# Kernel tuning notes

Hardware: AMD Instinct MI355X
Metric: run time of the kernel (lower is better)

## Reference

```python
import jax, jax.numpy as jnp
import numpy as np

TAO, M = 3, 5
C_IN, D_MODEL = 7, 512
KERNELS = D_MODEL // C_IN            # 73
LEFTOUT = D_MODEL - C_IN * KERNELS   # 1
KSIZE = 3
B, L = 32, 4096


def setup_inputs() -> dict:
    key = jax.random.key(0)
    k1, k2, k3, k4, k5 = jax.random.split(key, 5)
    x = jax.random.normal(k1, (B, L, C_IN), dtype=jnp.float32)
    fan_in = (M + 1) * KSIZE
    # kaiming_normal_(mode='fan_in', nonlinearity='leaky_relu', neg_slope=0.01)
    std = float(np.sqrt(2.0 / ((1.0 + 0.01 ** 2) * fan_in)))
    conv_w = jax.random.normal(k2, (KERNELS, M + 1, KSIZE), dtype=jnp.float32) * std
    bb = float(1.0 / np.sqrt(fan_in))  # torch default conv bias init: U(-1/sqrt(fan_in), +)
    conv_b = jax.random.uniform(k3, (KERNELS,), minval=-bb, maxval=bb, dtype=jnp.float32)
    leftout_w = jax.random.normal(k4, (LEFTOUT, M + 1, KSIZE), dtype=jnp.float32) * std
    leftout_b = jax.random.uniform(k5, (LEFTOUT,), minval=-bb, maxval=bb, dtype=jnp.float32)
    return {"x": x, "conv_w": conv_w, "conv_b": conv_b,
            "leftout_w": leftout_w, "leftout_b": leftout_b}


def _circ_conv(inp, w, b):
    # inp: [N, M+1, L]; circular padding=1, kernel 3, 'VALID' after wrap pad
    inp_c = jnp.pad(inp, ((0, 0), (0, 0), (1, 1)), mode="wrap")
    out = jax.lax.conv_general_dilated(
        inp_c, w, window_strides=(1,), padding="VALID",
        dimension_numbers=("NCH", "OIH", "NCH"))
    return out + b[None, :, None]


def reference(x, conv_w, conv_b, leftout_w, leftout_b):
    Bb, Ll, c = x.shape
    off = M * TAO
    # faithful-vector gather: for t in [off, L), take x[t - i*tao, c_], c-major then i
    idx = jnp.arange(off, Ll)[:, None] - jnp.arange(M + 1)[None, :] * TAO  # [L', M+1]
    g = x[:, idx, :]                                   # [B, L', M+1, c]
    g = jnp.transpose(g, (0, 1, 3, 2)).reshape(Bb, Ll - off, c * (M + 1))
    emb = jnp.pad(g, ((0, 0), (off, 0), (0, 0)))       # pad front of seq -> [B, L, c*(M+1)]
    # split into c chunks of (M+1) channels; fold chunk dim into batch for shared conv
    inp = emb.reshape(Bb, Ll, c, M + 1).transpose(0, 2, 3, 1).reshape(Bb * c, M + 1, Ll)
    out = _circ_conv(inp, conv_w, conv_b)              # [B*c, KERNELS, L]
    pieces = out.reshape(Bb, c * KERNELS, Ll)
    if LEFTOUT > 0:
        last = inp.reshape(Bb, c, M + 1, Ll)[:, -1]    # last chunk's conv input [B, M+1, L]
        extra = _circ_conv(last, leftout_w, leftout_b)  # [B, LEFTOUT, L]
        pieces = jnp.concatenate([pieces, extra], axis=1)
    return jnp.transpose(pieces, (0, 2, 1))            # [B, L, d_model]
```

## Files before the change

### kernel.cpp

```cpp
#include <hip/hip_runtime.h>

#define C_IN 7
#define D_MODEL 512
#define KERNELS 73
#define MM 5
#define BB 32
#define LL 4096
#define TCHUNK 256
#define NTAP 18

__global__ __launch_bounds__(512) void tokemb_kernel(
    const float* __restrict__ x, const float* __restrict__ conv_w,
    const float* __restrict__ conv_b, const float* __restrict__ leftout_w,
    const float* __restrict__ leftout_b, float* __restrict__ out)
{
  __shared__ float xs[(TCHUNK + NTAP) * C_IN];
  const int tid = threadIdx.x;
  const int b = blockIdx.y;
  const int T0 = blockIdx.x * TCHUNK;

  const int nelem = (TCHUNK + NTAP) * C_IN;
  const float* xb = x + (size_t)b * LL * C_IN;
  for (int e = tid; e < nelem; e += 512) {
    int q = e / C_IN;
    int r = e - q * C_IN;
    int p = T0 - 16 + q;
    if (p < 0) p += LL;
    else if (p >= LL) p -= LL;
    xs[e] = xb[p * C_IN + r];
  }

  const int d = tid;
  const bool left = (d == D_MODEL - 1);
  int cc, kk;
  if (left) { cc = C_IN - 1; kk = 0; }
  else { cc = d / KERNELS; kk = d - cc * KERNELS; }
  const float* wsrc = left ? leftout_w : (conv_w + kk * (MM + 1) * 3);
  float wf[NTAP];
  #pragma unroll
  for (int n = 0; n < NTAP; ++n) {
    int m = n / 3, j = 2 - (n % 3);
    wf[n] = wsrc[m * 3 + j];
  }
  const float bias = left ? leftout_b[0] : conv_b[kk];

  __syncthreads();

  float win[NTAP];
  #pragma unroll
  for (int n = 0; n < NTAP; ++n) win[n] = xs[(17 - n) * C_IN + cc];

  float* outb = out + ((size_t)b * LL + T0) * D_MODEL + d;

  for (int tl = 0; tl < TCHUNK; ++tl) {
    const int t = T0 + tl;
    float acc = bias;
    if (t >= 16 && t != LL - 1) {
      #pragma unroll
      for (int n = 0; n < NTAP; ++n) acc += win[n] * wf[n];
    } else {
      #pragma unroll
      for (int j = 0; j < 3; ++j) {
        int u = t - 1 + j;
        if (u < 0) u += LL;
        else if (u >= LL) u -= LL;
        if (u >= 15) {
          #pragma unroll
          for (int m = 0; m <= MM; ++m) {
            const int n = 3 * m + 2 - j;
            acc += win[n] * wf[n];
          }
        }
      }
    }
    outb[(size_t)tl * D_MODEL] = acc;
    #pragma unroll
    for (int n = NTAP - 1; n >= 1; --n) win[n] = win[n - 1];
    win[0] = xs[(tl + NTAP) * C_IN + cc];
  }
}

extern "C" void kernel_launch(void* const* d_in, const int* in_sizes, int n_in,
                              void* d_out, int out_size, void* d_ws, size_t ws_size,
                              hipStream_t stream) {
  const float* x = (const float*)d_in[0];
  const float* conv_w = (const float*)d_in[1];
  const float* conv_b = (const float*)d_in[2];
  const float* leftout_w = (const float*)d_in[3];
  const float* leftout_b = (const float*)d_in[4];
  float* out = (float*)d_out;
  dim3 grid(LL / TCHUNK, BB);
  tokemb_kernel<<<grid, 512, 0, stream>>>(x, conv_w, conv_b, leftout_w, leftout_b, out);
}
```

Before: 299.6 us.

## Shrink time chunks, store shared input channel-major, rotate register window by unrolling

The per-block time chunk drops from 256 to 72 steps, so the grid has far more blocks and fills the GPU better. The shared-memory staging buffer becomes channel-major, so each thread reads contiguous entries for its channel. The sliding window is no longer shifted by 17 register moves every step. Instead, the inner loop is unrolled 18 times with modulo indexing, so each new sample overwrites the oldest slot. In exchange, more halo samples are re-loaded per output, the boundary code path grows, and a tail guard is needed because 72 does not divide 4096.

```diff
diff --git a/kernel.cpp b/kernel.cpp
--- a/kernel.cpp
+++ b/kernel.cpp
@@ -4,30 +4,30 @@
 #define D_MODEL 512
 #define KERNELS 73
 #define MM 5
-#define BB 32
+#define BBATCH 32
 #define LL 4096
-#define TCHUNK 256
+#define TCHUNK 72
 #define NTAP 18
+#define XS_LD (TCHUNK + NTAP)
 
 __global__ __launch_bounds__(512) void tokemb_kernel(
     const float* __restrict__ x, const float* __restrict__ conv_w,
     const float* __restrict__ conv_b, const float* __restrict__ leftout_w,
     const float* __restrict__ leftout_b, float* __restrict__ out)
 {
-  __shared__ float xs[(TCHUNK + NTAP) * C_IN];
+  __shared__ float xs[C_IN * XS_LD];
   const int tid = threadIdx.x;
   const int b = blockIdx.y;
   const int T0 = blockIdx.x * TCHUNK;
 
-  const int nelem = (TCHUNK + NTAP) * C_IN;
   const float* xb = x + (size_t)b * LL * C_IN;
-  for (int e = tid; e < nelem; e += 512) {
-    int q = e / C_IN;
-    int r = e - q * C_IN;
+  for (int e = tid; e < C_IN * XS_LD; e += 512) {
+    int c = e / XS_LD;
+    int q = e - c * XS_LD;
     int p = T0 - 16 + q;
     if (p < 0) p += LL;
     else if (p >= LL) p -= LL;
-    xs[e] = xb[p * C_IN + r];
+    xs[e] = xb[p * C_IN + c];
   }
 
   const int d = tid;
@@ -46,37 +46,48 @@
 
   __syncthreads();
 
+  const float* xc = xs + cc * XS_LD;
+
   float win[NTAP];
   #pragma unroll
-  for (int n = 0; n < NTAP; ++n) win[n] = xs[(17 - n) * C_IN + cc];
+  for (int p = 0; p < NTAP; ++p) win[p] = xc[p];
 
   float* outb = out + ((size_t)b * LL + T0) * D_MODEL + d;
 
-  for (int tl = 0; tl < TCHUNK; ++tl) {
-    const int t = T0 + tl;
-    float acc = bias;
-    if (t >= 16 && t != LL - 1) {
+  for (int tl0 = 0; tl0 < TCHUNK; tl0 += NTAP) {
+    const int tg = T0 + tl0;
+    if (tg >= 16 && tg <= LL - 1 - NTAP) {
       #pragma unroll
-      for (int n = 0; n < NTAP; ++n) acc += win[n] * wf[n];
+      for (int u = 0; u < NTAP; ++u) {
+        float acc = bias;
+        #pragma unroll
+        for (int n = 0; n < NTAP; ++n)
+          acc += win[(u + 17 - n) % NTAP] * wf[n];
+        outb[(size_t)(tl0 + u) * D_MODEL] = acc;
+        win[u] = xc[tl0 + u + NTAP];
+      }
     } else {
       #pragma unroll
-      for (int j = 0; j < 3; ++j) {
-        int u = t - 1 + j;
-        if (u < 0) u += LL;
-        else if (u >= LL) u -= LL;
-        if (u >= 15) {
-          #pragma unroll
-          for (int m = 0; m <= MM; ++m) {
-            const int n = 3 * m + 2 - j;
-            acc += win[n] * wf[n];
+      for (int u = 0; u < NTAP; ++u) {
+        const int t = tg + u;
+        float acc = bias;
+        #pragma unroll
+        for (int j = 0; j < 3; ++j) {
+          int uu = t - 1 + j;
+          if (uu < 0) uu += LL;
+          else if (uu >= LL) uu -= LL;
+          if (uu >= 15) {
+            #pragma unroll
+            for (int m = 0; m <= MM; ++m) {
+              const int n = 3 * m + 2 - j;
+              acc += win[(u + 17 - n) % NTAP] * wf[n];
+            }
           }
         }
+        if (t < LL) outb[(size_t)(tl0 + u) * D_MODEL] = acc;
+        win[u] = xc[tl0 + u + NTAP];
       }
     }
-    outb[(size_t)tl * D_MODEL] = acc;
-    #pragma unroll
-    for (int n = NTAP - 1; n >= 1; --n) win[n] = win[n - 1];
-    win[0] = xs[(tl + NTAP) * C_IN + cc];
   }
 }
 
@@ -89,6 +100,6 @@
   const float* leftout_w = (const float*)d_in[3];
   const float* leftout_b = (const float*)d_in[4];
   float* out = (float*)d_out;
-  dim3 grid(LL / TCHUNK, BB);
+  dim3 grid((LL + TCHUNK - 1) / TCHUNK, BBATCH);
   tokemb_kernel<<<grid, 512, 0, stream>>>(x, conv_w, conv_b, leftout_w, leftout_b, out);
 }
```

Measured after the change: 280.7 us. 6.3% less time.
